# Optimization experiments

Hardware: AMD Instinct MI355X
Metric: run time of the kernel (lower is better)

## Reference

```python
import jax, jax.numpy as jnp
import numpy as np

DT = 0.1  # integration step
EPS = 1e-06

def setup_inputs() -> dict:
    key = jax.random.key(0)
    ks = jax.random.split(key, 8)
    B, T, I, H, O = 256, 512, 64, 512, 64
    return {
        'x_seq': jax.random.normal(ks[0], (B, T, I), jnp.float32),
        'W_in0': jax.random.normal(ks[1], (H, I), jnp.float32) * (1.0 / np.sqrt(I)),
        'b_in0': jnp.zeros((H,), jnp.float32),
        'A0':    jax.random.normal(ks[2], (H, H), jnp.float32) * 0.1,
        'tau0':  jnp.ones((H,), jnp.float32),
        'W_in1': jax.random.normal(ks[3], (H, H), jnp.float32) * (1.0 / np.sqrt(H)),
        'b_in1': jnp.zeros((H,), jnp.float32),
        'A1':    jax.random.normal(ks[4], (H, H), jnp.float32) * 0.1,
        'tau1':  jnp.ones((H,), jnp.float32),
        'W_out': jax.random.normal(ks[5], (O, H), jnp.float32) * (1.0 / np.sqrt(H)),
        'b_out': jnp.zeros((O,), jnp.float32),
    }

def _euler(h, drive, A, tau):
    # dh/dt = (1/|tau|+eps) * (-h + tanh(h @ A.T + drive)); Euler step
    inv_tau = 1.0 / (jnp.abs(tau) + EPS)
    dh = inv_tau * (-h + jnp.tanh(h @ A.T + drive))
    return h + DT * dh

def reference(x_seq, W_in0, b_in0, A0, tau0, W_in1, b_in1, A1, tau1, W_out, b_out):
    B, T, _ = x_seq.shape
    H = A0.shape[0]
    # layer-0 input projection is time-independent of hidden state: precompute
    xw = jnp.einsum('bti,hi->bth', x_seq, W_in0) + b_in0  # (B, T, H)

    def step(carry, xw_t):
        h0, h1 = carry
        h0 = _euler(h0, xw_t, A0, tau0)
        h1 = _euler(h1, h0 @ W_in1.T + b_in1, A1, tau1)
        y = h1 @ W_out.T + b_out
        return (h0, h1), y

    h0 = jnp.zeros((B, H), x_seq.dtype)
    h1 = jnp.zeros((B, H), x_seq.dtype)
    _, ys = jax.lax.scan(step, (h0, h1), jnp.swapaxes(xw, 0, 1))  # scan over time
    return jnp.swapaxes(ys, 0, 1)  # (B, T, O)
```

## Files before the change

### kernel.cpp

```cpp
#include <hip/hip_runtime.h>
#include <hip/hip_bf16.h>
#include <stdint.h>

#define B_ 256
#define T_ 512
#define I_ 64
#define H_ 512
#define O_ 64
#define DT_ 0.1f
#define EPS_ 1e-6f
#define SCALE_ 2048.0f
#define INVSCALE_ 4.8828125e-4f

typedef _Float16 f16x8 __attribute__((ext_vector_type(8)));
typedef float    f32x4 __attribute__((ext_vector_type(4)));

__device__ __forceinline__ f32x4 mfma16(f16x8 a, f16x8 b, f32x4 c) {
    return __builtin_amdgcn_mfma_f32_16x16x32_f16(a, b, c, 0, 0, 0);
}
__device__ __forceinline__ float fast_tanh(float x) {
    float e = __expf(2.0f * x);
    return 1.0f - 2.0f / (e + 1.0f);
}
__device__ __forceinline__ bool is_f32_input(const void* tau0) {
    return *(const unsigned int*)tau0 == 0x3F800000u;
}
__device__ __forceinline__ float load_any(const void* p, int i, bool f32) {
    return f32 ? ((const float*)p)[i] : (float)((const __bf16*)p)[i];
}
__device__ __forceinline__ _Float16 f16bits(unsigned short u) {
    union { unsigned short u; _Float16 f; } c; c.u = u; return c.f;
}
__device__ __forceinline__ unsigned short bits16(_Float16 f) {
    union { unsigned short u; _Float16 f; } c; c.f = f; return c.u;
}
__device__ __forceinline__ int bsum8(uint32_t v) {
    return (int)((v & 0xFF) + ((v >> 8) & 0xFF) + ((v >> 16) & 0xFF) + ((v >> 24) & 0xFF));
}
__device__ __forceinline__ int bmax8(uint32_t v) {
    int a = (int)(v & 0xFF), b = (int)((v >> 8) & 0xFF);
    int c = (int)((v >> 16) & 0xFF), d = (int)((v >> 24) & 0xFF);
    int x = a > b ? a : b, y = c > d ? c : d;
    return x > y ? x : y;
}

#define WS_A0H 0u
#define WS_A1H 524288u
#define WS_W1H 1048576u
#define WS_A0L 1572864u
#define WS_A1L 2097152u
#define WS_W1L 2621440u
#define WS_W0H 3145728u
#define WS_W0L 3211264u
#define WS_WOP 3276800u
#define WS_IT0 3407872u
#define WS_IT1 3409920u
#define WS_BI0 3411968u
#define WS_BI1 3414016u
#define WS_BO  3416064u
#define WS_FLGP 3538944u
#define WS_XCD2 3604480u
#define WS_HB0  4194304u
#define WS_HB1  6291456u

__global__ void k_swizzle(const void* __restrict__ src, _Float16* __restrict__ hi,
                          _Float16* __restrict__ lo, int NK, int kshift,
                          const void* __restrict__ tau) {
    bool f32 = is_f32_input(tau);
    int i = blockIdx.x * 256 + threadIdx.x;
    if (i >= NK) return;
    int n = i >> kshift;
    int k = i & ((1 << kshift) - 1);
    float v = load_any(src, i, f32);
    _Float16 h = (_Float16)v;
    _Float16 l = (_Float16)((v - (float)h) * SCALE_);
    int tile = n >> 4, m = n & 15, kk = k >> 5, q = (k >> 3) & 3, j = k & 7;
    int Kst = 1 << (kshift - 5);
    int off = ((tile * Kst + kk) << 9) + (((q << 4) | m) << 3) + j;
    hi[off] = h;
    lo[off] = l;
}

__global__ void k_swzwo(const void* __restrict__ src, _Float16* __restrict__ dst,
                        const void* __restrict__ tau) {
    bool f32 = is_f32_input(tau);
    int i = blockIdx.x * 256 + threadIdx.x;
    if (i >= 65536) return;
    int j = i & 7, l = (i >> 3) & 63, kk = (i >> 9) & 15, cg = i >> 13;
    int m = l & 15, q = l >> 4;
    int k = kk * 32 + q * 8 + j;
    float v = (m < 8) ? load_any(src, (8 * cg + m) * H_ + k, f32) : 0.0f;
    dst[i] = (_Float16)v;
}

__global__ void k_params(const void* t0, const void* t1,
                         const void* b0, const void* b1, const void* bo,
                         float* it0, float* it1, float* b0f, float* b1f, float* bof) {
    bool f32 = is_f32_input(t0);
    int i = threadIdx.x;
    if (i < H_) {
        it0[i] = 1.0f / (fabsf(load_any(t0, i, f32)) + EPS_);
        it1[i] = 1.0f / (fabsf(load_any(t1, i, f32)) + EPS_);
        b0f[i] = load_any(b0, i, f32);
        b1f[i] = load_any(b1, i, f32);
    }
    if (i < O_) bof[i] = load_any(bo, i, f32);
}

__global__ void k_zero(uint32_t* p, int n) {
    int i = blockIdx.x * 256 + threadIdx.x;
    if (i < n) p[i] = 0;
}

__device__ __forceinline__ void waitflag(const uint32_t* p, uint32_t tgt) {
    while (__hip_atomic_load(p, __ATOMIC_RELAXED, __HIP_MEMORY_SCOPE_AGENT) < tgt) { }
    __asm__ __volatile__("" ::: "memory");
}

__global__ __launch_bounds__(256, 1) void liquid_kernel(
    const void* __restrict__ x_seq, const void* __restrict__ tau0probe,
    char* __restrict__ ws, void* __restrict__ out)
{
    __shared__ _Float16 hTh[2][16][520], hTl[2][16][520];
    __shared__ float yscr[4][16][16];
    __shared__ int s_fast;

    const bool f32 = is_f32_input(tau0probe);
    const int tid  = threadIdx.x;
    const int lane = tid & 63;
    const int w    = tid >> 6;
    const int m    = lane & 15;
    const int q    = lane >> 4;
    const int koff = q * 8;
    const int rg   = blockIdx.x;
    const int cg   = blockIdx.y;
    const int chain = blockIdx.z;
    const int r0   = rg * 16;
    const int colg = cg * 64 + w * 16 + m;
    const int tlg  = cg * 4 + w;
    const int c0   = w * 128 + lane;
    const int c1   = c0 + 64;

    uint32_t* ring = (uint32_t*)(ws + WS_HB0);
    uint32_t* hb1  = (uint32_t*)(ws + WS_HB1);
    uint32_t* fpad = (uint32_t*)(ws + WS_FLGP);
    uint32_t* fsf  = fpad +         (size_t)rg * 8 * 32;
    uint32_t* f1f  = fpad + 4096  + (size_t)rg * 8 * 32;
    uint32_t* pg1  = fpad + 12288 + (size_t)rg * 8 * 32;

    {
        uint32_t* xc = (uint32_t*)(ws + WS_XCD2) + (size_t)rg * 32;
        if (tid == 0) {
            int xid = (int)(__builtin_amdgcn_s_getreg((3u << 11) | 20u) & 7u);
            __hip_atomic_fetch_add(xc + (xid >> 2), 1u << (8 * (xid & 3)),
                                   __ATOMIC_RELAXED, __HIP_MEMORY_SCOPE_AGENT);
            uint32_t v0, v1;
            do {
                __builtin_amdgcn_s_sleep(1);
                v0 = __hip_atomic_load(xc,     __ATOMIC_RELAXED, __HIP_MEMORY_SCOPE_AGENT);
                v1 = __hip_atomic_load(xc + 1, __ATOMIC_RELAXED, __HIP_MEMORY_SCOPE_AGENT);
            } while (bsum8(v0) + bsum8(v1) < 16);
            int mx0 = bmax8(v0), mx1 = bmax8(v1);
            s_fast = ((mx0 > mx1 ? mx0 : mx1) == 16) ? 1 : 0;
        }
    }

    const float* bow = (const float*)(ws + WS_BO);
    const float boY  = (m < 8) ? bow[cg * 8 + m] : 0.0f;

    __syncthreads();
    const bool fastp = (s_fast != 0);

    if (chain == 0) {
        const float it0c = ((const float*)(ws + WS_IT0))[colg];
        const float bi0c = ((const float*)(ws + WS_BI0))[colg];
        const size_t fb  = (((size_t)(tlg * 16)) << 9) + (lane << 3);
        const size_t fb0 = (((size_t)(tlg * 2))  << 9) + (lane << 3);
        f16x8 cA0h[16], cA0l[16];
#pragma unroll
        for (int kk = 0; kk < 16; ++kk) {
            cA0h[kk] = *(const f16x8*)((const _Float16*)(ws + WS_A0H) + fb + ((size_t)kk << 9));
            cA0l[kk] = *(const f16x8*)((const _Float16*)(ws + WS_A0L) + fb + ((size_t)kk << 9));
        }
        f16x8 cW0h[2], cW0l[2];
#pragma unroll
        for (int kk = 0; kk < 2; ++kk) {
            cW0h[kk] = *(const f16x8*)((const _Float16*)(ws + WS_W0H) + fb0 + ((size_t)kk << 9));
            cW0l[kk] = *(const f16x8*)((const _Float16*)(ws + WS_W0L) + fb0 + ((size_t)kk << 9));
        }
        const float*  xpf = (const float*) x_seq + (size_t)(r0 + m) * T_ * I_ + koff;
        const __bf16* xpb = (const __bf16*)x_seq + (size_t)(r0 + m) * T_ * I_ + koff;
        float h0m[4] = {0.f, 0.f, 0.f, 0.f};

        f32x4 xf0 = {}, xf1 = {}, xf2 = {}, xf3 = {};
        uint4 xb0 = {}, xb1 = {};
        if (f32) {
            xf0 = *(const f32x4*)(xpf);
            xf1 = *(const f32x4*)(xpf + 4);
            xf2 = *(const f32x4*)(xpf + 32);
            xf3 = *(const f32x4*)(xpf + 36);
        } else {
            xb0 = *(const uint4*)(xpb);
            xb1 = *(const uint4*)(xpb + 32);
        }

        for (int s = 0; s < T_; ++s) {
            const int cur = s & 1;
            const int rs4 = s & 3;
            const int ws4 = (s + 1) & 3;

            waitflag(fsf + (size_t)(2 * w) * 32,     4u * (uint32_t)s);
            waitflag(fsf + (size_t)(2 * w + 1) * 32, 4u * (uint32_t)s);
            uint32_t rv0[16], rv1[16];
            {
                const uint32_t* src = ring + ((size_t)(rs4 * 16 + rg) * 16) * 512;
                if (fastp) {
#pragma unroll
                    for (int k = 0; k < 16; ++k) {
                        rv0[k] = src[(size_t)k * 512 + c0];
                        rv1[k] = src[(size_t)k * 512 + c1];
                    }
                } else {
#pragma unroll
                    for (int k = 0; k < 16; ++k) {
                        rv0[k] = __hip_atomic_load(src + (size_t)k * 512 + c0, __ATOMIC_RELAXED, __HIP_MEMORY_SCOPE_AGENT);
                        rv1[k] = __hip_atomic_load(src + (size_t)k * 512 + c1, __ATOMIC_RELAXED, __HIP_MEMORY_SCOPE_AGENT);
                    }
                }
            }
#pragma unroll
            for (int k = 0; k < 16; ++k) {
                hTh[cur][k][c0] = f16bits((unsigned short)(rv0[k] & 0xFFFFu));
                hTl[cur][k][c0] = f16bits((unsigned short)(rv0[k] >> 16));
                hTh[cur][k][c1] = f16bits((unsigned short)(rv1[k] & 0xFFFFu));
                hTl[cur][k][c1] = f16bits((unsigned short)(rv1[k] >> 16));
            }
            __syncthreads();

            f32x4 a1 = {0.f,0.f,0.f,0.f}, a2 = {0.f,0.f,0.f,0.f}, a3 = {0.f,0.f,0.f,0.f};
#pragma unroll
            for (int kk = 0; kk < 16; ++kk) {
                f16x8 ah = *(const f16x8*)(&hTh[cur][m][kk * 32 + koff]);
                f16x8 al = *(const f16x8*)(&hTl[cur][m][kk * 32 + koff]);
                a1 = mfma16(ah, cA0h[kk], a1);
                a2 = mfma16(ah, cA0l[kk], a2);
                a3 = mfma16(al, cA0h[kk], a3);
            }
            {
                f16x8 xh0, xl0, xh1, xl1;
                if (f32) {
                    float v0[8] = {xf0[0],xf0[1],xf0[2],xf0[3],xf1[0],xf1[1],xf1[2],xf1[3]};
                    float v1[8] = {xf2[0],xf2[1],xf2[2],xf2[3],xf3[0],xf3[1],xf3[2],xf3[3]};
#pragma unroll
                    for (int j = 0; j < 8; ++j) {
                        xh0[j] = (_Float16)v0[j];
                        xl0[j] = (_Float16)((v0[j] - (float)xh0[j]) * SCALE_);
                        xh1[j] = (_Float16)v1[j];
                        xl1[j] = (_Float16)((v1[j] - (float)xh1[j]) * SCALE_);
                    }
                } else {
                    const __bf16* p0 = (const __bf16*)&xb0;
                    const __bf16* p1 = (const __bf16*)&xb1;
#pragma unroll
                    for (int j = 0; j < 8; ++j) {
                        xh0[j] = (_Float16)(float)p0[j]; xl0[j] = (_Float16)0.0f;
                        xh1[j] = (_Float16)(float)p1[j]; xl1[j] = (_Float16)0.0f;
                    }
                }
                a1 = mfma16(xh0, cW0h[0], a1);
                a2 = mfma16(xh0, cW0l[0], a2);
                a3 = mfma16(xl0, cW0h[0], a3);
                a1 = mfma16(xh1, cW0h[1], a1);
                a2 = mfma16(xh1, cW0l[1], a2);
                a3 = mfma16(xl1, cW0h[1], a3);
            }

            if (s >= 3) {
                const uint32_t tgt = 4u * (uint32_t)(s - 3);
                const uint32_t* pp = pg1 + (size_t)(lane & 7) * 32;
                uint32_t v = (lane < 8)
                    ? __hip_atomic_load(pp, __ATOMIC_RELAXED, __HIP_MEMORY_SCOPE_AGENT)
                    : 0xFFFFFFFFu;
                while (__any(v < tgt)) {
                    v = (lane < 8)
                        ? __hip_atomic_load(pp, __ATOMIC_RELAXED, __HIP_MEMORY_SCOPE_AGENT)
                        : 0xFFFFFFFFu;
                }
                __asm__ __volatile__("" ::: "memory");
            }

            uint32_t* dst = ring + ((size_t)(ws4 * 16 + rg) * 16) * 512 + colg;
#pragma unroll
            for (int r = 0; r < 4; ++r) {
                float z = a1[r] + (a2[r] + a3[r]) * INVSCALE_ + bi0c;
                float h = h0m[r];
                h += DT_ * it0c * (fast_tanh(z) - h);
                h0m[r] = h;
                _Float16 hh = (_Float16)h;
                _Float16 hl = (_Float16)((h - (float)hh) * SCALE_);
                uint32_t pk = (uint32_t)bits16(hh) | ((uint32_t)bits16(hl) << 16);
                if (fastp) dst[(size_t)(q * 4 + r) * 512] = pk;
                else __hip_atomic_store(dst + (size_t)(q * 4 + r) * 512, pk,
                                        __ATOMIC_RELAXED, __HIP_MEMORY_SCOPE_AGENT);
            }
            asm volatile("s_waitcnt vmcnt(0)" ::: "memory");
            if (lane == 0)
                __hip_atomic_fetch_add(fsf + (size_t)cg * 32, 1u, __ATOMIC_RELAXED, __HIP_MEMORY_SCOPE_AGENT);

            {
                const int tn = (s + 1 < T_) ? s + 1 : s;
                if (f32) {
                    const float* p = xpf + (size_t)tn * I_;
                    xf0 = *(const f32x4*)(p);
                    xf1 = *(const f32x4*)(p + 4);
                    xf2 = *(const f32x4*)(p + 32);
                    xf3 = *(const f32x4*)(p + 36);
                } else {
                    const __bf16* p = xpb + (size_t)tn * I_;
                    xb0 = *(const uint4*)(p);
                    xb1 = *(const uint4*)(p + 32);
                }
            }
        }
        return;
    }

    {
        const float it1c = ((const float*)(ws + WS_IT1))[colg];
        const float bi1c = ((const float*)(ws + WS_BI1))[colg];
        const size_t fb = (((size_t)(tlg * 16)) << 9) + (lane << 3);
        f16x8 cA1h[16], cA1l[16], cW1h[16], cW1l[16];
#pragma unroll
        for (int kk = 0; kk < 16; ++kk) {
            cA1h[kk] = *(const f16x8*)((const _Float16*)(ws + WS_A1H) + fb + ((size_t)kk << 9));
            cA1l[kk] = *(const f16x8*)((const _Float16*)(ws + WS_A1L) + fb + ((size_t)kk << 9));
            cW1h[kk] = *(const f16x8*)((const _Float16*)(ws + WS_W1H) + fb + ((size_t)kk << 9));
            cW1l[kk] = *(const f16x8*)((const _Float16*)(ws + WS_W1L) + fb + ((size_t)kk << 9));
        }
        const _Float16* pWOP = (const _Float16*)(ws + WS_WOP) + (((size_t)(cg * 16)) << 9) + (lane << 3);
        float h1m[4] = {0.f, 0.f, 0.f, 0.f};

        for (int s = 0; s < T_; ++s) {
            const int cur = s & 1, nxt = (s + 1) & 1;
            const int rs4 = (s + 1) & 3;

            waitflag(f1f + (size_t)(2 * w) * 32,     4u * (uint32_t)s);
            waitflag(f1f + (size_t)(2 * w + 1) * 32, 4u * (uint32_t)s);
            uint32_t rv0[16], rv1[16];
            {
                const uint32_t* src = hb1 + ((size_t)(cur * 16 + rg) * 16) * 512;
                if (fastp) {
#pragma unroll
                    for (int k = 0; k < 16; ++k) {
                        rv0[k] = src[(size_t)k * 512 + c0];
                        rv1[k] = src[(size_t)k * 512 + c1];
                    }
                } else {
#pragma unroll
                    for (int k = 0; k < 16; ++k) {
                        rv0[k] = __hip_atomic_load(src + (size_t)k * 512 + c0, __ATOMIC_RELAXED, __HIP_MEMORY_SCOPE_AGENT);
                        rv1[k] = __hip_atomic_load(src + (size_t)k * 512 + c1, __ATOMIC_RELAXED, __HIP_MEMORY_SCOPE_AGENT);
                    }
                }
            }
            waitflag(fsf + (size_t)(2 * w) * 32,     4u * (uint32_t)(s + 1));
            waitflag(fsf + (size_t)(2 * w + 1) * 32, 4u * (uint32_t)(s + 1));
#pragma unroll
            for (int k = 0; k < 16; ++k) {
                hTh[0][k][c0] = f16bits((unsigned short)(rv0[k] & 0xFFFFu));
                hTl[0][k][c0] = f16bits((unsigned short)(rv0[k] >> 16));
                hTh[0][k][c1] = f16bits((unsigned short)(rv1[k] & 0xFFFFu));
                hTl[0][k][c1] = f16bits((unsigned short)(rv1[k] >> 16));
            }
            __syncthreads();

            {
                const uint32_t* src = ring + ((size_t)(rs4 * 16 + rg) * 16) * 512;
                if (fastp) {
#pragma unroll
                    for (int k = 0; k < 16; ++k) {
                        rv0[k] = src[(size_t)k * 512 + c0];
                        rv1[k] = src[(size_t)k * 512 + c1];
                    }
                } else {
#pragma unroll
                    for (int k = 0; k < 16; ++k) {
                        rv0[k] = __hip_atomic_load(src + (size_t)k * 512 + c0, __ATOMIC_RELAXED, __HIP_MEMORY_SCOPE_AGENT);
                        rv1[k] = __hip_atomic_load(src + (size_t)k * 512 + c1, __ATOMIC_RELAXED, __HIP_MEMORY_SCOPE_AGENT);
                    }
                }
            }

            if (s >= 1) {
                f32x4 y1 = {0.f,0.f,0.f,0.f}, y2 = {0.f,0.f,0.f,0.f};
#pragma unroll
                for (int kk2 = 0; kk2 < 4; ++kk2) {
                    int kk = w * 4 + kk2;
                    f16x8 ah = *(const f16x8*)(&hTh[0][m][kk * 32 + koff]);
                    f16x8 al = *(const f16x8*)(&hTl[0][m][kk * 32 + koff]);
                    f16x8 b  = *(const f16x8*)(pWOP + ((size_t)kk << 9));
                    y1 = mfma16(ah, b, y1);
                    y2 = mfma16(al, b, y2);
                }
#pragma unroll
                for (int r = 0; r < 4; ++r)
                    yscr[w][q * 4 + r][m] = y1[r] + y2[r] * INVSCALE_;
            }

            f32x4 a1 = {0.f,0.f,0.f,0.f}, a2 = {0.f,0.f,0.f,0.f}, a3 = {0.f,0.f,0.f,0.f};
#pragma unroll
            for (int kk = 0; kk < 16; ++kk) {
                f16x8 ah = *(const f16x8*)(&hTh[0][m][kk * 32 + koff]);
                f16x8 al = *(const f16x8*)(&hTl[0][m][kk * 32 + koff]);
                a1 = mfma16(ah, cA1h[kk], a1);
                a2 = mfma16(ah, cA1l[kk], a2);
                a3 = mfma16(al, cA1h[kk], a3);
            }

#pragma unroll
            for (int k = 0; k < 16; ++k) {
                hTh[1][k][c0] = f16bits((unsigned short)(rv0[k] & 0xFFFFu));
                hTl[1][k][c0] = f16bits((unsigned short)(rv0[k] >> 16));
                hTh[1][k][c1] = f16bits((unsigned short)(rv1[k] & 0xFFFFu));
                hTl[1][k][c1] = f16bits((unsigned short)(rv1[k] >> 16));
            }
            if (lane == 0)
                __hip_atomic_fetch_add(pg1 + (size_t)cg * 32, 1u, __ATOMIC_RELAXED, __HIP_MEMORY_SCOPE_AGENT);
            __syncthreads();

#pragma unroll
            for (int kk = 0; kk < 16; ++kk) {
                f16x8 ah = *(const f16x8*)(&hTh[1][m][kk * 32 + koff]);
                f16x8 al = *(const f16x8*)(&hTl[1][m][kk * 32 + koff]);
                a1 = mfma16(ah, cW1h[kk], a1);
                a2 = mfma16(ah, cW1l[kk], a2);
                a3 = mfma16(al, cW1h[kk], a3);
            }

            uint32_t* dst = hb1 + ((size_t)(nxt * 16 + rg) * 16) * 512 + colg;
#pragma unroll
            for (int r = 0; r < 4; ++r) {
                float z = a1[r] + (a2[r] + a3[r]) * INVSCALE_ + bi1c;
                float h = h1m[r];
                h += DT_ * it1c * (fast_tanh(z) - h);
                h1m[r] = h;
                _Float16 hh = (_Float16)h;
                _Float16 hl = (_Float16)((h - (float)hh) * SCALE_);
                uint32_t pk = (uint32_t)bits16(hh) | ((uint32_t)bits16(hl) << 16);
                if (fastp) dst[(size_t)(q * 4 + r) * 512] = pk;
                else __hip_atomic_store(dst + (size_t)(q * 4 + r) * 512, pk,
                                        __ATOMIC_RELAXED, __HIP_MEMORY_SCOPE_AGENT);
            }
            asm volatile("s_waitcnt vmcnt(0)" ::: "memory");
            if (lane == 0)
                __hip_atomic_fetch_add(f1f + (size_t)cg * 32, 1u, __ATOMIC_RELAXED, __HIP_MEMORY_SCOPE_AGENT);

            if (w == 0 && s >= 1 && m < 8) {
#pragma unroll
                for (int r = 0; r < 4; ++r) {
                    float v = yscr[0][q * 4 + r][m] + yscr[1][q * 4 + r][m]
                            + yscr[2][q * 4 + r][m] + yscr[3][q * 4 + r][m] + boY;
                    size_t idx = ((size_t)(r0 + q * 4 + r) * T_ + (s - 1)) * O_ + cg * 8 + m;
                    if (f32) ((float*)out)[idx] = v;
                    else     ((__bf16*)out)[idx] = (__bf16)v;
                }
            }
        }

        waitflag(f1f + (size_t)(2 * w) * 32,     4u * (uint32_t)T_);
        waitflag(f1f + (size_t)(2 * w + 1) * 32, 4u * (uint32_t)T_);
        {
            uint32_t rv0[16], rv1[16];
            const uint32_t* src = hb1 + ((size_t)((T_ & 1) * 16 + rg) * 16) * 512;
            if (fastp) {
#pragma unroll
                for (int k = 0; k < 16; ++k) {
                    rv0[k] = src[(size_t)k * 512 + c0];
                    rv1[k] = src[(size_t)k * 512 + c1];
                }
            } else {
#pragma unroll
                for (int k = 0; k < 16; ++k) {
                    rv0[k] = __hip_atomic_load(src + (size_t)k * 512 + c0, __ATOMIC_RELAXED, __HIP_MEMORY_SCOPE_AGENT);
                    rv1[k] = __hip_atomic_load(src + (size_t)k * 512 + c1, __ATOMIC_RELAXED, __HIP_MEMORY_SCOPE_AGENT);
                }
            }
            __syncthreads();
#pragma unroll
            for (int k = 0; k < 16; ++k) {
                hTh[0][k][c0] = f16bits((unsigned short)(rv0[k] & 0xFFFFu));
                hTl[0][k][c0] = f16bits((unsigned short)(rv0[k] >> 16));
                hTh[0][k][c1] = f16bits((unsigned short)(rv1[k] & 0xFFFFu));
                hTl[0][k][c1] = f16bits((unsigned short)(rv1[k] >> 16));
            }
        }
        __syncthreads();
        {
            f32x4 y1 = {0.f,0.f,0.f,0.f}, y2 = {0.f,0.f,0.f,0.f};
#pragma unroll
            for (int kk2 = 0; kk2 < 4; ++kk2) {
                int kk = w * 4 + kk2;
                f16x8 ah = *(const f16x8*)(&hTh[0][m][kk * 32 + koff]);
                f16x8 al = *(const f16x8*)(&hTl[0][m][kk * 32 + koff]);
                f16x8 b  = *(const f16x8*)(pWOP + ((size_t)kk << 9));
                y1 = mfma16(ah, b, y1);
                y2 = mfma16(al, b, y2);
            }
#pragma unroll
            for (int r = 0; r < 4; ++r)
                yscr[w][q * 4 + r][m] = y1[r] + y2[r] * INVSCALE_;
        }
        __syncthreads();
        if (w == 0 && m < 8) {
#pragma unroll
            for (int r = 0; r < 4; ++r) {
                float v = yscr[0][q * 4 + r][m] + yscr[1][q * 4 + r][m]
                        + yscr[2][q * 4 + r][m] + yscr[3][q * 4 + r][m] + boY;
                size_t idx = ((size_t)(r0 + q * 4 + r) * T_ + (T_ - 1)) * O_ + cg * 8 + m;
                if (f32) ((float*)out)[idx] = v;
                else     ((__bf16*)out)[idx] = (__bf16)v;
            }
        }
    }
}

extern "C" void kernel_launch(void* const* d_in, const int* in_sizes, int n_in,
                              void* d_out, int out_size, void* d_ws, size_t ws_size,
                              hipStream_t stream) {
    const void* x_seq = d_in[0];
    const void* W_in0 = d_in[1];
    const void* b_in0 = d_in[2];
    const void* A0    = d_in[3];
    const void* tau0  = d_in[4];
    const void* W_in1 = d_in[5];
    const void* b_in1 = d_in[6];
    const void* A1    = d_in[7];
    const void* tau1  = d_in[8];
    const void* W_out = d_in[9];
    const void* b_out = d_in[10];

    char* ws = (char*)d_ws;
    const int HH = H_ * H_, HI = H_ * I_;

    k_swizzle<<<(HH + 255) / 256, 256, 0, stream>>>(A0,    (_Float16*)(ws + WS_A0H), (_Float16*)(ws + WS_A0L), HH, 9, tau0);
    k_swizzle<<<(HH + 255) / 256, 256, 0, stream>>>(A1,    (_Float16*)(ws + WS_A1H), (_Float16*)(ws + WS_A1L), HH, 9, tau0);
    k_swizzle<<<(HH + 255) / 256, 256, 0, stream>>>(W_in1, (_Float16*)(ws + WS_W1H), (_Float16*)(ws + WS_W1L), HH, 9, tau0);
    k_swizzle<<<(HI + 255) / 256, 256, 0, stream>>>(W_in0, (_Float16*)(ws + WS_W0H), (_Float16*)(ws + WS_W0L), HI, 6, tau0);
    k_swzwo <<<65536 / 256, 256, 0, stream>>>(W_out, (_Float16*)(ws + WS_WOP), tau0);
    k_params<<<1, 512, 0, stream>>>(tau0, tau1, b_in0, b_in1, b_out,
                                    (float*)(ws + WS_IT0), (float*)(ws + WS_IT1),
                                    (float*)(ws + WS_BI0), (float*)(ws + WS_BI1),
                                    (float*)(ws + WS_BO));
    k_zero<<<(16896 + 255) / 256, 256, 0, stream>>>((uint32_t*)(ws + WS_FLGP), 16896);
    k_zero<<<(786432 + 255) / 256, 256, 0, stream>>>((uint32_t*)(ws + WS_HB0), 786432);

    liquid_kernel<<<dim3(16, 8, 2), dim3(256), 0, stream>>>(x_seq, tau0, ws, d_out);
}
```

Before: 3.056 ms.

## Replace atomic-add counters with per-wave step flags and whole-wave polling

Inter-block step counters that every wave incremented with fetch_add become per-wave slots. Each wave stores its own step index into its slot, and consumers poll all 32 slots (8 groups × 4 waves) at once using the wave's lanes with __any. This removes atomic RMW contention on shared counters and lets one vector load check every producer. The cost is that each wait now covers all column groups, not only the two it previously checked, so waits may become stricter and wait on unrelated producers.

```diff
diff --git a/kernel.cpp b/kernel.cpp
--- a/kernel.cpp
+++ b/kernel.cpp
@@ -112,8 +112,16 @@
     if (i < n) p[i] = 0;
 }
 
-__device__ __forceinline__ void waitflag(const uint32_t* p, uint32_t tgt) {
-    while (__hip_atomic_load(p, __ATOMIC_RELAXED, __HIP_MEMORY_SCOPE_AGENT) < tgt) { }
+__device__ __forceinline__ void pollall(const uint32_t* base, uint32_t tgt, int lane) {
+    const uint32_t* p = base + (size_t)(lane >> 2) * 32 + (lane & 3);
+    uint32_t v = (lane < 32)
+        ? __hip_atomic_load(p, __ATOMIC_RELAXED, __HIP_MEMORY_SCOPE_AGENT)
+        : 0xFFFFFFFFu;
+    while (__any(v < tgt)) {
+        v = (lane < 32)
+            ? __hip_atomic_load(p, __ATOMIC_RELAXED, __HIP_MEMORY_SCOPE_AGENT)
+            : 0xFFFFFFFFu;
+    }
     __asm__ __volatile__("" ::: "memory");
 }
 
@@ -209,8 +217,7 @@
             const int rs4 = s & 3;
             const int ws4 = (s + 1) & 3;
 
-            waitflag(fsf + (size_t)(2 * w) * 32,     4u * (uint32_t)s);
-            waitflag(fsf + (size_t)(2 * w + 1) * 32, 4u * (uint32_t)s);
+            pollall(fsf, (uint32_t)s, lane);
             uint32_t rv0[16], rv1[16];
             {
                 const uint32_t* src = ring + ((size_t)(rs4 * 16 + rg) * 16) * 512;
@@ -276,17 +283,7 @@
             }
 
             if (s >= 3) {
-                const uint32_t tgt = 4u * (uint32_t)(s - 3);
-                const uint32_t* pp = pg1 + (size_t)(lane & 7) * 32;
-                uint32_t v = (lane < 8)
-                    ? __hip_atomic_load(pp, __ATOMIC_RELAXED, __HIP_MEMORY_SCOPE_AGENT)
-                    : 0xFFFFFFFFu;
-                while (__any(v < tgt)) {
-                    v = (lane < 8)
-                        ? __hip_atomic_load(pp, __ATOMIC_RELAXED, __HIP_MEMORY_SCOPE_AGENT)
-                        : 0xFFFFFFFFu;
-                }
-                __asm__ __volatile__("" ::: "memory");
+                pollall(pg1, (uint32_t)(s - 3), lane);
             }
 
             uint32_t* dst = ring + ((size_t)(ws4 * 16 + rg) * 16) * 512 + colg;
@@ -305,7 +302,8 @@
             }
             asm volatile("s_waitcnt vmcnt(0)" ::: "memory");
             if (lane == 0)
-                __hip_atomic_fetch_add(fsf + (size_t)cg * 32, 1u, __ATOMIC_RELAXED, __HIP_MEMORY_SCOPE_AGENT);
+                __hip_atomic_store(fsf + (size_t)cg * 32 + w, (uint32_t)(s + 1),
+                                   __ATOMIC_RELAXED, __HIP_MEMORY_SCOPE_AGENT);
 
             {
                 const int tn = (s + 1 < T_) ? s + 1 : s;
@@ -344,8 +342,7 @@
             const int cur = s & 1, nxt = (s + 1) & 1;
             const int rs4 = (s + 1) & 3;
 
-            waitflag(f1f + (size_t)(2 * w) * 32,     4u * (uint32_t)s);
-            waitflag(f1f + (size_t)(2 * w + 1) * 32, 4u * (uint32_t)s);
+            pollall(f1f, (uint32_t)s, lane);
             uint32_t rv0[16], rv1[16];
             {
                 const uint32_t* src = hb1 + ((size_t)(cur * 16 + rg) * 16) * 512;
@@ -363,8 +360,7 @@
                     }
                 }
             }
-            waitflag(fsf + (size_t)(2 * w) * 32,     4u * (uint32_t)(s + 1));
-            waitflag(fsf + (size_t)(2 * w + 1) * 32, 4u * (uint32_t)(s + 1));
+            pollall(fsf, (uint32_t)(s + 1), lane);
 #pragma unroll
             for (int k = 0; k < 16; ++k) {
                 hTh[0][k][c0] = f16bits((unsigned short)(rv0[k] & 0xFFFFu));
@@ -425,7 +421,8 @@
                 hTl[1][k][c1] = f16bits((unsigned short)(rv1[k] >> 16));
             }
             if (lane == 0)
-                __hip_atomic_fetch_add(pg1 + (size_t)cg * 32, 1u, __ATOMIC_RELAXED, __HIP_MEMORY_SCOPE_AGENT);
+                __hip_atomic_store(pg1 + (size_t)cg * 32 + w, (uint32_t)(s + 1),
+                                   __ATOMIC_RELAXED, __HIP_MEMORY_SCOPE_AGENT);
             __syncthreads();
 
 #pragma unroll
@@ -453,7 +450,8 @@
             }
             asm volatile("s_waitcnt vmcnt(0)" ::: "memory");
             if (lane == 0)
-                __hip_atomic_fetch_add(f1f + (size_t)cg * 32, 1u, __ATOMIC_RELAXED, __HIP_MEMORY_SCOPE_AGENT);
+                __hip_atomic_store(f1f + (size_t)cg * 32 + w, (uint32_t)(s + 1),
+                                   __ATOMIC_RELAXED, __HIP_MEMORY_SCOPE_AGENT);
 
             if (w == 0 && s >= 1 && m < 8) {
 #pragma unroll
@@ -467,8 +465,7 @@
             }
         }
 
-        waitflag(f1f + (size_t)(2 * w) * 32,     4u * (uint32_t)T_);
-        waitflag(f1f + (size_t)(2 * w + 1) * 32, 4u * (uint32_t)T_);
+        pollall(f1f, (uint32_t)T_, lane);
         {
             uint32_t rv0[16], rv1[16];
             const uint32_t* src = hb1 + ((size_t)((T_ & 1) * 16 + rg) * 16) * 512;
```

After: 2.829 ms. -7.4%, faster.
